# Kernel optimization log

Measured on AMD Instinct MI355X. Metric: run time of the kernel, lower is better.

The kernel has to match this reference:

```python
import jax, jax.numpy as jnp
import numpy as np

N, S, D = 2, 2048, 512
HEADS, HEAD_DIM = 8, 64
SCALE_BASE = 512.0
EPS = 1e-08


def xpos_apply(x, positions, downscale):
    # x: (B, S, d)  positions: (B, S) float
    d = x.shape[-1]
    half = jnp.arange(0, d, 2, dtype=jnp.float32)
    scale_vec = (half + 0.4 * d) / (1.4 * d)                      # (d/2,)
    power = positions[..., None] / SCALE_BASE                     # (B, S, 1)
    scale = scale_vec ** power                                    # (B, S, d/2)
    inv_freq = 1.0 / (10000.0 ** (half / d))                      # (d/2,)
    sinusoid = positions[..., None] * inv_freq                    # (B, S, d/2)
    sin = jnp.sin(sinusoid)
    cos = jnp.cos(sinusoid)
    if downscale:
        scale = 1.0 / scale
    # duplicate-interleave to full dim
    sin = jnp.repeat(sin, 2, axis=-1)
    cos = jnp.repeat(cos, 2, axis=-1)
    scale = jnp.repeat(scale, 2, axis=-1)
    x1 = x[..., 0::2]
    x2 = x[..., 1::2]
    rot = jnp.stack([-x2, x1], axis=-1).reshape(x.shape)          # rotate_every_two
    return (x * cos + rot * sin) * scale


def split_heads(x):
    # (N, S, H*Hd) -> (N*H, S, Hd)
    return x.reshape(N, S, HEADS, HEAD_DIM).transpose(0, 2, 1, 3).reshape(N * HEADS, S, HEAD_DIM)


def setup_inputs() -> dict:
    key = jax.random.key(0)
    ks = jax.random.split(key, 8)
    g = 1.0 / np.sqrt(D)
    return {
        'sequence': jax.random.normal(ks[0], (N, S, D), dtype=jnp.float32),
        'input_mask': jnp.ones((N, S), dtype=jnp.float32),
        'positions': jnp.tile(jnp.arange(S, dtype=jnp.int32), (N, 1)),
        'layer_num': 0,
        'Wq': jax.random.normal(ks[1], (D, D), dtype=jnp.float32) * g,
        'bq': jnp.zeros((D,), dtype=jnp.float32),
        'Wk': jax.random.normal(ks[2], (D, D), dtype=jnp.float32) * g,
        'bk': jnp.zeros((D,), dtype=jnp.float32),
        'Wv': jax.random.normal(ks[3], (D, D), dtype=jnp.float32) * g,
        'bv': jnp.zeros((D,), dtype=jnp.float32),
        'Wo': jax.random.normal(ks[4], (D, D), dtype=jnp.float32) * g,
        'bo': jnp.zeros((D,), dtype=jnp.float32),
    }


def reference(sequence, input_mask, positions, layer_num, Wq, bq, Wk, bk, Wv, bv, Wo, bo):
    scaling = HEAD_DIM ** (-0.5)
    posf = positions.astype(jnp.float32)

    Q = split_heads(sequence @ Wq.T + bq) * scaling               # (N*H, S, Hd)
    K = split_heads(sequence @ Wk.T + bk)
    V = split_heads(sequence @ Wv.T + bv)

    pos_h = jnp.repeat(posf, HEADS, axis=0)                       # 'n s -> (n h) s'
    K = xpos_apply(K, pos_h, downscale=True)
    Q = xpos_apply(Q, pos_h, downscale=False)

    A = jnp.einsum('nsd,ntd->nst', Q, K).reshape(N, HEADS, S, S)  # (N, H, S, S2)
    Vh = V.reshape(N, HEADS, S, HEAD_DIM)

    # causal mask: input_mask over kv dim, lower-triangular
    tri = jnp.tril(jnp.ones((S, S), dtype=jnp.float32))
    attn_mask = input_mask[:, None, None, :] * tri[None, None]    # (N, 1, S, S2)

    A = jax.nn.sigmoid(A) * attn_mask

    # stick-breaking decay: reverse-cumprod of (1 - A) along kv dim, shifted
    Af = jnp.flip(A, axis=(2, 3))
    C = jnp.exp(jnp.cumsum(jnp.log(1.0 - Af + EPS), axis=-1))
    C = jnp.flip(C, axis=(2, 3))
    C = jnp.concatenate([jnp.ones((N, HEADS, S, 1), dtype=C.dtype), C[..., :-1]], axis=-1)

    A = C * A
    attended = jnp.einsum('nhst,nhtd->nhsd', A, Vh)               # (N, H, S, Hd)
    attended = attended.transpose(0, 2, 1, 3).reshape(N, S, HEADS * HEAD_DIM)
    out = attended @ Wo.T + bo
    return out
```

## Files before the change

### kernel.cpp

```cpp
#include <hip/hip_runtime.h>
#include <math.h>

#define S_LEN 2048
#define DMODEL 512
#define HDIM 64
#define EPS_G 1e-8f

typedef __bf16 bf16x8 __attribute__((ext_vector_type(8)));
typedef __bf16 bf16x4 __attribute__((ext_vector_type(4)));
typedef float f32x4 __attribute__((ext_vector_type(4)));

template <int CTRL>
__device__ __forceinline__ float dpp_mov(float src, float oldv) {
  return __int_as_float(__builtin_amdgcn_update_dpp(
      __float_as_int(oldv), __float_as_int(src), CTRL, 0xF, 0xF, false));
}
#define ROW_SHL(n) (0x100 + (n))
#define ROW_SHR(n) (0x110 + (n))

__device__ __forceinline__ float swz_head(float v) {
  return __int_as_float(__builtin_amdgcn_ds_swizzle(__float_as_int(v), 0x0010));
}
__device__ __forceinline__ float swz_tail(float v) {
  return __int_as_float(__builtin_amdgcn_ds_swizzle(__float_as_int(v), 0x01F0));
}

__global__ __launch_bounds__(256) void cvt_kernel(
    const float* __restrict__ X, const float* __restrict__ Wq,
    const float* __restrict__ Wk, const float* __restrict__ Wv,
    const float* __restrict__ Wo,
    __bf16* __restrict__ Xb, __bf16* __restrict__ Wb, __bf16* __restrict__ Wob) {
  const int u = blockIdx.x * 256 + threadIdx.x;
  const float* src; __bf16* dst; int off;
  if (u < 524288)      { src = X;  dst = Xb;          off = u; }
  else if (u < 589824) { src = Wq; dst = Wb;          off = u - 524288; }
  else if (u < 655360) { src = Wk; dst = Wb + 262144; off = u - 589824; }
  else if (u < 720896) { src = Wv; dst = Wb + 524288; off = u - 655360; }
  else                 { src = Wo; dst = Wob;         off = u - 720896; }
  const float4 v = *(const float4*)(src + (size_t)off * 4);
  bf16x4 o;
  o[0] = (__bf16)v.x; o[1] = (__bf16)v.y; o[2] = (__bf16)v.z; o[3] = (__bf16)v.w;
  *(bf16x4*)(dst + (size_t)off * 4) = o;
}

__global__ __launch_bounds__(256, 2) void qkv_gemm(
    const __bf16* __restrict__ Xb, const __bf16* __restrict__ Wb,
    const float* __restrict__ bq, const float* __restrict__ bk, const float* __restrict__ bv,
    const int* __restrict__ pos,
    __bf16* __restrict__ Qh, __bf16* __restrict__ Kh, __bf16* __restrict__ Vt) {
  const int i0 = blockIdx.x << 6;
  const int h  = blockIdx.y;
  const int j0 = h << 6;

  __shared__ __bf16 Xs[64][72];
  __shared__ __bf16 Wls[3][64][72];

  const int tid = threadIdx.x;
  const int wv = tid >> 6, lane = tid & 63;
  const int l = lane & 15, seg = lane >> 4;
  const int sr = tid >> 2, sc = (tid & 3) << 4;

  f32x4 O[3][4];
#pragma unroll
  for (int w = 0; w < 3; ++w)
#pragma unroll
    for (int r4 = 0; r4 < 4; ++r4) O[w][r4] = (f32x4){0.f, 0.f, 0.f, 0.f};

  bf16x8 xr0, xr1, wr[3][2];
#define LOADQKV(K0)                                                                   \
  {                                                                                   \
    const __bf16* xp = Xb + (size_t)(i0 + sr) * 512 + (K0) + sc;                      \
    xr0 = *(const bf16x8*)xp; xr1 = *(const bf16x8*)(xp + 8);                         \
    _Pragma("unroll")                                                                 \
    for (int w = 0; w < 3; ++w) {                                                     \
      const __bf16* wp = Wb + (size_t)w * 262144 + (size_t)(j0 + sr) * 512 + (K0) + sc;\
      wr[w][0] = *(const bf16x8*)wp; wr[w][1] = *(const bf16x8*)(wp + 8);             \
    }                                                                                 \
  }

  LOADQKV(0)
  for (int k0 = 0; k0 < 512; k0 += 64) {
    __syncthreads();
    *(bf16x8*)&Xs[sr][sc]     = xr0;
    *(bf16x8*)&Xs[sr][sc + 8] = xr1;
#pragma unroll
    for (int w = 0; w < 3; ++w) {
      *(bf16x8*)&Wls[w][sr][sc]     = wr[w][0];
      *(bf16x8*)&Wls[w][sr][sc + 8] = wr[w][1];
    }
    __syncthreads();
    if (k0 < 448) LOADQKV(k0 + 64)

    bf16x8 a0[4], a1[4];
#pragma unroll
    for (int r4 = 0; r4 < 4; ++r4) {
      a0[r4] = *(const bf16x8*)&Xs[r4 * 16 + l][seg * 8];
      a1[r4] = *(const bf16x8*)&Xs[r4 * 16 + l][seg * 8 + 32];
    }
#pragma unroll
    for (int w = 0; w < 3; ++w) {
      bf16x8 b0 = *(const bf16x8*)&Wls[w][wv * 16 + l][seg * 8];
      bf16x8 b1 = *(const bf16x8*)&Wls[w][wv * 16 + l][seg * 8 + 32];
#pragma unroll
      for (int r4 = 0; r4 < 4; ++r4) {
        O[w][r4] = __builtin_amdgcn_mfma_f32_16x16x32_bf16(a0[r4], b0, O[w][r4], 0, 0, 0);
        O[w][r4] = __builtin_amdgcn_mfma_f32_16x16x32_bf16(a1[r4], b1, O[w][r4], 0, 0, 0);
      }
    }
  }

  const int d = wv * 16 + l;
  const float bbq = bq[j0 + d], bbk = bk[j0 + d], bbv = bv[j0 + d];
#pragma unroll
  for (int r4 = 0; r4 < 4; ++r4)
#pragma unroll
    for (int reg = 0; reg < 4; ++reg) {
      O[0][r4][reg] += bbq; O[1][r4][reg] += bbk; O[2][r4][reg] += bbv;
    }

  const int n = i0 >> 11, sb = i0 & 2047;
  const int nh = (n << 3) + h;

  const float kp   = (float)(d >> 1);
  const float invf = exp2f(-0.41524100f * kp) * 0.15915494f;
  const float l2sv = log2f((2.f * kp + 25.6f) * (1.f / 89.6f));
  float pv_[4][4];
#pragma unroll
  for (int r4 = 0; r4 < 4; ++r4)
#pragma unroll
    for (int reg = 0; reg < 4; ++reg)
      pv_[r4][reg] = (float)pos[n * S_LEN + sb + r4 * 16 + (seg << 2) + reg];

  __syncthreads();

#pragma unroll
  for (int r4 = 0; r4 < 4; ++r4)
#pragma unroll
    for (int reg = 0; reg < 4; ++reg) {
      const int row = r4 * 16 + (seg << 2) + reg;
      const float p = pv_[r4][reg];
      const float rev0 = p * invf;
      const float rev  = rev0 - floorf(rev0);
      const float sn = __builtin_amdgcn_sinf(rev);
      const float cn = __builtin_amdgcn_cosf(rev);
      const float sq = exp2f(p * (1.f / 512.f) * l2sv);
      const float sQ = sq * 0.125f;
      const float sK = __builtin_amdgcn_rcpf(sq);
      float x  = O[0][r4][reg];
      float xp = __shfl_xor(x, 1);
      Xs[row][d] = (__bf16)((((d & 1) ? (x * cn + xp * sn) : (x * cn - xp * sn))) * sQ);
      x  = O[1][r4][reg];
      xp = __shfl_xor(x, 1);
      Wls[0][row][d] = (__bf16)((((d & 1) ? (x * cn + xp * sn) : (x * cn - xp * sn))) * sK);
      Wls[1][row][d] = (__bf16)O[2][r4][reg];
    }
  __syncthreads();

  __bf16* qdst = Qh + (((size_t)nh * S_LEN + sb + sr) << 6) + sc;
  *(bf16x8*)qdst       = *(bf16x8*)&Xs[sr][sc];
  *(bf16x8*)(qdst + 8) = *(bf16x8*)&Xs[sr][sc + 8];
  __bf16* kdst = Kh + (((size_t)nh * S_LEN + sb + sr) << 6) + sc;
  *(bf16x8*)kdst       = *(bf16x8*)&Wls[0][sr][sc];
  *(bf16x8*)(kdst + 8) = *(bf16x8*)&Wls[0][sr][sc + 8];

  const int dv = tid >> 2, part = tid & 3;
  __bf16 tmp[16];
#pragma unroll
  for (int i = 0; i < 16; ++i) tmp[i] = Wls[1][part * 16 + i][dv];
  __bf16* vdst = Vt + (((size_t)(nh * 64 + dv)) << 11) + sb + part * 16;
  *(bf16x8*)vdst       = *(bf16x8*)&tmp[0];
  *(bf16x8*)(vdst + 8) = *(bf16x8*)&tmp[8];
}

__global__ __launch_bounds__(256, 2) void attn_chunk(
    const __bf16* __restrict__ Qh, const __bf16* __restrict__ Kh,
    const __bf16* __restrict__ Vt, const float* __restrict__ imask,
    __bf16* __restrict__ att, float* __restrict__ PartO,
    float* __restrict__ PartP, float* __restrict__ PartA0) {
  const int id = blockIdx.x;
  const int nh = id & 15;
  const int t  = id >> 4;
  int rb, c, nc;
  if (t < 8)       { rb = t; c = 0; nc = 1; }
  else if (t < 24) { int u = t - 8;  rb = 8  + (u >> 1); c = u & 1;     nc = 2; }
  else if (t < 48) { int u = t - 24; rb = 16 + u / 3;    c = u - 3 * (u / 3); nc = 3; }
  else             { int u = t - 48; rb = 24 + (u >> 2); c = u & 3;     nc = 4; }
  const int hi = rb - (c << 3);
  const int lo = (c == nc - 1) ? 0 : hi - 7;

  const int n = nh >> 3, h = nh & 7;
  const int tid = threadIdx.x;
  const int wv = tid >> 6, lane = tid & 63;
  const int l = lane & 15, seg = lane >> 4;
  const int pr = tid >> 3, pc = (tid & 7) << 3;

  __shared__ __bf16 Qs16[64][72];
  __shared__ __bf16 Ks16[64][72];
  __shared__ __bf16 Vt16[64][72];
  __shared__ __bf16 cs16[64][72];
  __shared__ float msk[64];

  for (int idx = tid; idx < 512; idx += 256) {
    int r = idx >> 3, c8 = (idx & 7) << 3;
    *(bf16x8*)&Qs16[r][c8] =
        *(const bf16x8*)(Qh + (((size_t)nh * S_LEN + rb * 64 + r) << 6) + c8);
  }

  f32x4 O[4];
  float pend[4][4];
  float Crow[4];
  float a0k0[4];
#pragma unroll
  for (int nt = 0; nt < 4; ++nt) O[nt] = (f32x4){0.f, 0.f, 0.f, 0.f};
#pragma unroll
  for (int r = 0; r < 4; ++r) {
    Crow[r] = 1.f; a0k0[r] = 0.f;
#pragma unroll
    for (int nt = 0; nt < 4; ++nt) pend[r][nt] = 0.f;
  }

  bf16x8 kp0, kp1, vp0, vp1;
  float mp = 0.f;
#define LOADKV(JT)                                                                     \
  kp0 = *(const bf16x8*)(Kh + (((size_t)nh * S_LEN + (JT) * 64 + pr) << 6) + pc);      \
  kp1 = *(const bf16x8*)(Kh + (((size_t)nh * S_LEN + (JT) * 64 + 32 + pr) << 6) + pc); \
  vp0 = *(const bf16x8*)(Vt + (((size_t)(nh * 64 + pr)) << 11) + (JT) * 64 + pc);      \
  vp1 = *(const bf16x8*)(Vt + (((size_t)(nh * 64 + 32 + pr)) << 11) + (JT) * 64 + pc); \
  if (tid < 64) mp = imask[n * S_LEN + (JT) * 64 + tid];

  LOADKV(hi)

  for (int jt = hi; jt >= lo; --jt) {
    __syncthreads();
    *(bf16x8*)&Ks16[pr][pc]      = kp0;
    *(bf16x8*)&Ks16[32 + pr][pc] = kp1;
    *(bf16x8*)&Vt16[pr][pc]      = vp0;
    *(bf16x8*)&Vt16[32 + pr][pc] = vp1;
    if (tid < 64) msk[tid] = mp;
    __syncthreads();
    if (jt > lo) { LOADKV(jt - 1) }

    bf16x8 aq0 = *(const bf16x8*)&Qs16[wv * 16 + l][seg * 8];
    bf16x8 aq1 = *(const bf16x8*)&Qs16[wv * 16 + l][seg * 8 + 32];
    f32x4 Sv[4];
#pragma unroll
    for (int nt = 0; nt < 4; ++nt) {
      bf16x8 bk0 = *(const bf16x8*)&Ks16[nt * 16 + l][seg * 8];
      bf16x8 bk1 = *(const bf16x8*)&Ks16[nt * 16 + l][seg * 8 + 32];
      f32x4 z = (f32x4){0.f, 0.f, 0.f, 0.f};
      z = __builtin_amdgcn_mfma_f32_16x16x32_bf16(aq0, bk0, z, 0, 0, 0);
      z = __builtin_amdgcn_mfma_f32_16x16x32_bf16(aq1, bk1, z, 0, 0, 0);
      Sv[nt] = z;
    }

    float v0f[4];
#pragma unroll
    for (int nt = 0; nt < 4; ++nt) v0f[nt] = (float)Vt16[nt * 16 + l][0];

#pragma unroll
    for (int reg = 0; reg < 4; ++reg) {
      const int qrow = rb * 64 + wv * 16 + seg * 4 + reg;
      float a_[4], f_[4], p_[4];
#pragma unroll
      for (int nt = 0; nt < 4; ++nt) {
        const int key = jt * 64 + nt * 16 + l;
        const float s = Sv[nt][reg];
        const float mv = msk[nt * 16 + l];
        const float av = (key <= qrow)
            ? mv * __builtin_amdgcn_rcpf(1.f + __expf(-s))
            : 0.f;
        a_[nt] = av;
        f_[nt] = 1.f - av + EPS_G;
      }
#pragma unroll
      for (int nt = 0; nt < 4; ++nt) {
        float p = f_[nt];
        p *= dpp_mov<ROW_SHL(1)>(p, 1.f);
        p *= dpp_mov<ROW_SHL(2)>(p, 1.f);
        p *= dpp_mov<ROW_SHL(4)>(p, 1.f);
        p *= dpp_mov<ROW_SHL(8)>(p, 1.f);
        p_[nt] = p;
      }
      float P_[4], tl[4];
#pragma unroll
      for (int nt = 0; nt < 4; ++nt) {
        P_[nt] = swz_head(p_[nt]);
        tl[nt] = swz_tail(f_[nt]);
      }
      const float a0 = swz_head(a_[0]);
      const float T3 = 1.f, T2 = P_[3], T1 = T2 * P_[2], T0 = T1 * P_[1];
      const float Tarr[4] = {T0, T1, T2, T3};
      const float Ptile = T0 * P_[0];
      const float crow = Crow[reg];
#pragma unroll
      for (int nt = 0; nt < 4; ++nt) {
        const float pprev = dpp_mov<ROW_SHR(1)>(p_[nt], 0.f);
        float cv;
        if (l > 0)
          cv = a_[nt] * pprev * Tarr[nt] * crow;
        else if (nt > 0)
          cv = a_[nt] * tl[nt - 1] * P_[nt] * Tarr[nt] * crow;
        else
          cv = (jt == 0 && nc == 1) ? a_[0] : 0.f;
        cs16[wv * 16 + seg * 4 + reg][nt * 16 + l] = (__bf16)cv;
      }
      if (jt == 0) a0k0[reg] = a0;
      const float f63 = tl[3];
      const float s0  = a0 * Ptile * crow;
      Crow[reg] = crow * Ptile;
#pragma unroll
      for (int nt = 0; nt < 4; ++nt) {
        O[nt][reg] += pend[reg][nt] * f63;
        pend[reg][nt] = s0 * v0f[nt];
      }
    }

    bf16x8 ac0 = *(const bf16x8*)&cs16[wv * 16 + l][seg * 8];
    bf16x8 ac1 = *(const bf16x8*)&cs16[wv * 16 + l][seg * 8 + 32];
#pragma unroll
    for (int nt = 0; nt < 4; ++nt) {
      bf16x8 bv0 = *(const bf16x8*)&Vt16[nt * 16 + l][seg * 8];
      bf16x8 bv1 = *(const bf16x8*)&Vt16[nt * 16 + l][seg * 8 + 32];
      O[nt] = __builtin_amdgcn_mfma_f32_16x16x32_bf16(ac0, bv0, O[nt], 0, 0, 0);
      O[nt] = __builtin_amdgcn_mfma_f32_16x16x32_bf16(ac1, bv1, O[nt], 0, 0, 0);
    }
  }

  if (lo > 0) {
    const int m = lo << 6;
    const float mb = imask[n * S_LEN + m - 1];
    const __bf16* kb = Kh + (((size_t)nh * S_LEN + m - 1) << 6) + seg * 16;
    bf16x8 kb0 = *(const bf16x8*)kb, kb1 = *(const bf16x8*)(kb + 8);
    bf16x8 q0 = *(const bf16x8*)&Qs16[wv * 16 + l][seg * 16];
    bf16x8 q1 = *(const bf16x8*)&Qs16[wv * 16 + l][seg * 16 + 8];
    float sc_ = 0.f;
#pragma unroll
    for (int j = 0; j < 8; ++j)
      sc_ += (float)q0[j] * (float)kb0[j] + (float)q1[j] * (float)kb1[j];
    sc_ += __shfl_xor(sc_, 16);
    sc_ += __shfl_xor(sc_, 32);
    const float fbl = 1.f - mb * __builtin_amdgcn_rcpf(1.f + __expf(-sc_)) + EPS_G;
#pragma unroll
    for (int reg = 0; reg < 4; ++reg) {
      const float fb = __shfl(fbl, (seg << 2) + reg);
#pragma unroll
      for (int nt = 0; nt < 4; ++nt) O[nt][reg] += pend[reg][nt] * fb;
    }
  }

  if (nc == 1) {
#pragma unroll
    for (int nt = 0; nt < 4; ++nt)
#pragma unroll
      for (int reg = 0; reg < 4; ++reg) {
        const int srow = rb * 64 + wv * 16 + seg * 4 + reg;
        att[((size_t)(n * S_LEN + srow)) * DMODEL + h * HDIM + nt * 16 + l] =
            (__bf16)O[nt][reg];
      }
  } else {
    const int slot = nh * 72 + (t - 8);
    float* po = PartO + (size_t)slot * 4096;
#pragma unroll
    for (int nt = 0; nt < 4; ++nt)
#pragma unroll
      for (int reg = 0; reg < 4; ++reg)
        po[(wv * 16 + seg * 4 + reg) * 64 + nt * 16 + l] = O[nt][reg];
    if (l == 0) {
#pragma unroll
      for (int reg = 0; reg < 4; ++reg)
        PartP[slot * 64 + wv * 16 + seg * 4 + reg] = Crow[reg];
      if (lo == 0) {
#pragma unroll
        for (int reg = 0; reg < 4; ++reg)
          PartA0[(nh * 24 + rb - 8) * 64 + wv * 16 + seg * 4 + reg] = a0k0[reg];
      }
    }
  }
}

__global__ __launch_bounds__(256) void combine_kernel(
    const float* __restrict__ PartO, const float* __restrict__ PartP,
    const float* __restrict__ PartA0, const __bf16* __restrict__ Vt,
    __bf16* __restrict__ att) {
  const int b = blockIdx.x;
  const int nh = b / 24;
  const int rb = 8 + (b - nh * 24);
  const int nc = (rb < 16) ? 2 : ((rb < 24) ? 3 : 4);
  const int t0 = (rb < 16) ? 8 + ((rb - 8) << 1)
               : (rb < 24) ? 24 + (rb - 16) * 3
                           : 48 + ((rb - 24) << 2);
  const int n = nh >> 3, h = nh & 7;
  const int tid = threadIdx.x;
  const int r = tid >> 2, db = (tid & 3) << 4;

  float acc[16];
#pragma unroll
  for (int j = 0; j < 16; ++j) acc[j] = 0.f;
  float fac = 1.f;
  for (int c = 0; c < nc; ++c) {
    const int slot = nh * 72 + (t0 - 8) + c;
    const float* po = PartO + (size_t)slot * 4096 + r * 64 + db;
    const float P = PartP[slot * 64 + r];
#pragma unroll
    for (int q = 0; q < 4; ++q) {
      const float4 v = *(const float4*)(po + q * 4);
      acc[q * 4 + 0] += fac * v.x; acc[q * 4 + 1] += fac * v.y;
      acc[q * 4 + 2] += fac * v.z; acc[q * 4 + 3] += fac * v.w;
    }
    fac *= P;
  }
  const float a0 = PartA0[(nh * 24 + rb - 8) * 64 + r];
#pragma unroll
  for (int j = 0; j < 16; ++j)
    acc[j] += a0 * (float)Vt[(((size_t)(nh * 64 + db + j)) << 11)];

  __bf16 ob[16];
#pragma unroll
  for (int j = 0; j < 16; ++j) ob[j] = (__bf16)acc[j];
  __bf16* dst = att + ((size_t)(n * S_LEN + rb * 64 + r)) * DMODEL + h * HDIM + db;
  *(bf16x8*)dst       = *(bf16x8*)&ob[0];
  *(bf16x8*)(dst + 8) = *(bf16x8*)&ob[8];
}

__global__ __launch_bounds__(256, 2) void out_gemm(const __bf16* __restrict__ Xa,
                                                   const __bf16* __restrict__ Wob,
                                                   const float* __restrict__ bo,
                                                   float* __restrict__ Out) {
  const int i0 = blockIdx.x << 6, j0 = blockIdx.y << 7;
  __shared__ __bf16 As[64][72];
  __shared__ __bf16 Bs[128][72];

  const int tid = threadIdx.x;
  const int wv = tid >> 6, lane = tid & 63;
  const int l = lane & 15, seg = lane >> 4;
  const int sr = tid >> 2, sc = (tid & 3) << 4;

  f32x4 O[2][4];
#pragma unroll
  for (int j = 0; j < 2; ++j)
#pragma unroll
    for (int r4 = 0; r4 < 4; ++r4) O[j][r4] = (f32x4){0.f, 0.f, 0.f, 0.f};

  bf16x8 ar0, ar1, br[2][2];
#define LOADOUT(K0)                                                          \
  {                                                                          \
    const __bf16* xp = Xa + (size_t)(i0 + sr) * 512 + (K0) + sc;             \
    ar0 = *(const bf16x8*)xp; ar1 = *(const bf16x8*)(xp + 8);                \
    _Pragma("unroll")                                                        \
    for (int ps = 0; ps < 2; ++ps) {                                         \
      const __bf16* wp = Wob + (size_t)(j0 + ps * 64 + sr) * 512 + (K0) + sc;\
      br[ps][0] = *(const bf16x8*)wp; br[ps][1] = *(const bf16x8*)(wp + 8);  \
    }                                                                        \
  }

  LOADOUT(0)
  for (int k0 = 0; k0 < 512; k0 += 64) {
    __syncthreads();
    *(bf16x8*)&As[sr][sc]     = ar0;
    *(bf16x8*)&As[sr][sc + 8] = ar1;
#pragma unroll
    for (int ps = 0; ps < 2; ++ps) {
      *(bf16x8*)&Bs[ps * 64 + sr][sc]     = br[ps][0];
      *(bf16x8*)&Bs[ps * 64 + sr][sc + 8] = br[ps][1];
    }
    __syncthreads();
    if (k0 < 448) LOADOUT(k0 + 64)

    bf16x8 a0[4], a1[4];
#pragma unroll
    for (int r4 = 0; r4 < 4; ++r4) {
      a0[r4] = *(const bf16x8*)&As[r4 * 16 + l][seg * 8];
      a1[r4] = *(const bf16x8*)&As[r4 * 16 + l][seg * 8 + 32];
    }
#pragma unroll
    for (int j = 0; j < 2; ++j) {
      const int u = wv + 4 * j;
      bf16x8 b0 = *(const bf16x8*)&Bs[u * 16 + l][seg * 8];
      bf16x8 b1 = *(const bf16x8*)&Bs[u * 16 + l][seg * 8 + 32];
#pragma unroll
      for (int r4 = 0; r4 < 4; ++r4) {
        O[j][r4] = __builtin_amdgcn_mfma_f32_16x16x32_bf16(a0[r4], b0, O[j][r4], 0, 0, 0);
        O[j][r4] = __builtin_amdgcn_mfma_f32_16x16x32_bf16(a1[r4], b1, O[j][r4], 0, 0, 0);
      }
    }
  }

#pragma unroll
  for (int j = 0; j < 2; ++j) {
    const int u = wv + 4 * j;
    const float bb = bo[j0 + u * 16 + l];
#pragma unroll
    for (int r4 = 0; r4 < 4; ++r4)
#pragma unroll
      for (int reg = 0; reg < 4; ++reg) {
        const int m = r4 * 16 + (seg << 2) + reg;
        Out[(size_t)(i0 + m) * 512 + j0 + u * 16 + l] = O[j][r4][reg] + bb;
      }
  }
}

extern "C" void kernel_launch(void* const* d_in, const int* in_sizes, int n_in,
                              void* d_out, int out_size, void* d_ws, size_t ws_size,
                              hipStream_t stream) {
  (void)in_sizes; (void)n_in; (void)out_size; (void)ws_size;
  const float* seq  = (const float*)d_in[0];
  const float* mask = (const float*)d_in[1];
  const int*   pos  = (const int*)d_in[2];
  const float* Wq = (const float*)d_in[4];
  const float* bq = (const float*)d_in[5];
  const float* Wk = (const float*)d_in[6];
  const float* bk = (const float*)d_in[7];
  const float* Wv = (const float*)d_in[8];
  const float* bv = (const float*)d_in[9];
  const float* Wo = (const float*)d_in[10];
  const float* bo = (const float*)d_in[11];
  float* out = (float*)d_out;

  char* base = (char*)d_ws;
  __bf16* att = (__bf16*)base;
  __bf16* Qh  = (__bf16*)(base + ( 4u << 20));
  __bf16* Kh  = (__bf16*)(base + ( 8u << 20));
  __bf16* Vt  = (__bf16*)(base + (12u << 20));
  __bf16* Wb  = (__bf16*)(base + (16u << 20));
  __bf16* Wob = (__bf16*)(base + (18u << 20));
  __bf16* Xb  = (__bf16*)(base + (19u << 20));
  float* PartO  = (float*)(base + (23u << 20));
  float* PartP  = (float*)(base + (42u << 20));
  float* PartA0 = (float*)(base + (43u << 20));

  cvt_kernel<<<3072, 256, 0, stream>>>(seq, Wq, Wk, Wv, Wo, Xb, Wb, Wob);
  qkv_gemm<<<dim3(64, 8), 256, 0, stream>>>(Xb, Wb, bq, bk, bv, pos, Qh, Kh, Vt);
  attn_chunk<<<1280, 256, 0, stream>>>(Qh, Kh, Vt, mask, att, PartO, PartP, PartA0);
  combine_kernel<<<384, 256, 0, stream>>>(PartO, PartP, PartA0, Vt, att);
  out_gemm<<<dim3(64, 4), 256, 0, stream>>>(att, Wob, bo, out);
}
```

Measured before the change: 168.8 us.

## Balance chunk split, reverse block order, raise occupancy, streamline mask math

Measured after the change: 159.9 us. 1.06x faster.

```diff
diff --git a/kernel.cpp b/kernel.cpp
--- a/kernel.cpp
+++ b/kernel.cpp
@@ -172,12 +172,12 @@
   *(bf16x8*)(vdst + 8) = *(bf16x8*)&tmp[8];
 }
 
-__global__ __launch_bounds__(256, 2) void attn_chunk(
+__global__ __launch_bounds__(256, 4) void attn_chunk(
     const __bf16* __restrict__ Qh, const __bf16* __restrict__ Kh,
     const __bf16* __restrict__ Vt, const float* __restrict__ imask,
     __bf16* __restrict__ att, float* __restrict__ PartO,
     float* __restrict__ PartP, float* __restrict__ PartA0) {
-  const int id = blockIdx.x;
+  const int id = 1279 - (int)blockIdx.x;
   const int nh = id & 15;
   const int t  = id >> 4;
   int rb, c, nc;
@@ -185,8 +185,13 @@
   else if (t < 24) { int u = t - 8;  rb = 8  + (u >> 1); c = u & 1;     nc = 2; }
   else if (t < 48) { int u = t - 24; rb = 16 + u / 3;    c = u - 3 * (u / 3); nc = 3; }
   else             { int u = t - 48; rb = 24 + (u >> 2); c = u & 3;     nc = 4; }
-  const int hi = rb - (c << 3);
-  const int lo = (c == nc - 1) ? 0 : hi - 7;
+  const int T   = rb + 1;
+  const int bsz = T / nc;
+  const int rem = T - bsz * nc;
+  const int szc  = bsz + ((c < rem) ? 1 : 0);
+  const int skip = c * bsz + ((c < rem) ? c : rem);
+  const int hi = rb - skip;
+  const int lo = hi - szc + 1;
 
   const int n = nh >> 3, h = nh & 7;
   const int tid = threadIdx.x;
@@ -257,21 +262,29 @@
 #pragma unroll
     for (int nt = 0; nt < 4; ++nt) v0f[nt] = (float)Vt16[nt * 16 + l][0];
 
+    float mv_[4];
+#pragma unroll
+    for (int nt = 0; nt < 4; ++nt) mv_[nt] = msk[nt * 16 + l];
+
+    const bool diag  = (jt == rb);
+    const int  kbase = jt * 64 + l;
+
 #pragma unroll
     for (int reg = 0; reg < 4; ++reg) {
       const int qrow = rb * 64 + wv * 16 + seg * 4 + reg;
       float a_[4], f_[4], p_[4];
 #pragma unroll
       for (int nt = 0; nt < 4; ++nt) {
-        const int key = jt * 64 + nt * 16 + l;
         const float s = Sv[nt][reg];
-        const float mv = msk[nt * 16 + l];
-        const float av = (key <= qrow)
-            ? mv * __builtin_amdgcn_rcpf(1.f + __expf(-s))
-            : 0.f;
-        a_[nt] = av;
-        f_[nt] = 1.f - av + EPS_G;
-      }
+        a_[nt] = mv_[nt] * __builtin_amdgcn_rcpf(1.f + __expf(-s));
+      }
+      if (diag) {
+#pragma unroll
+        for (int nt = 0; nt < 4; ++nt)
+          if (kbase + nt * 16 > qrow) a_[nt] = 0.f;
+      }
+#pragma unroll
+      for (int nt = 0; nt < 4; ++nt) f_[nt] = 1.f - a_[nt] + EPS_G;
 #pragma unroll
       for (int nt = 0; nt < 4; ++nt) {
         float p = f_[nt];
@@ -288,20 +301,16 @@
         tl[nt] = swz_tail(f_[nt]);
       }
       const float a0 = swz_head(a_[0]);
-      const float T3 = 1.f, T2 = P_[3], T1 = T2 * P_[2], T0 = T1 * P_[1];
-      const float Tarr[4] = {T0, T1, T2, T3};
+      const float crow = Crow[reg];
+      const float T2 = P_[3], T1 = T2 * P_[2], T0 = T1 * P_[1];
+      const float TC[4] = {T0 * crow, T1 * crow, T2 * crow, crow};
       const float Ptile = T0 * P_[0];
-      const float crow = Crow[reg];
 #pragma unroll
       for (int nt = 0; nt < 4; ++nt) {
-        const float pprev = dpp_mov<ROW_SHR(1)>(p_[nt], 0.f);
-        float cv;
-        if (l > 0)
-          cv = a_[nt] * pprev * Tarr[nt] * crow;
-        else if (nt > 0)
-          cv = a_[nt] * tl[nt - 1] * P_[nt] * Tarr[nt] * crow;
-        else
-          cv = (jt == 0 && nc == 1) ? a_[0] : 0.f;
+        const float bnd = (nt == 0) ? 0.f : tl[nt - 1] * P_[nt];
+        const float sel = dpp_mov<ROW_SHR(1)>(p_[nt], bnd);
+        float cv = a_[nt] * sel * TC[nt];
+        if (nt == 0 && jt == 0 && nc == 1 && l == 0) cv = a_[0];
         cs16[wv * 16 + seg * 4 + reg][nt * 16 + l] = (__bf16)cv;
       }
       if (jt == 0) a0k0[reg] = a0;
```
